# Kernel optimization log

Hardware: AMD Instinct MI355X
Metric: run time of the kernel (lower is better)

The kernel has to match this reference:

```python
import jax, jax.numpy as jnp
import numpy as np

B, S, V, E, P, C = 256, 128, 32000, 300, 200, 3
DIST_CUTOFF = 10

def _seq_mask(x):
    # TF: count_nonzero over seq, sequence_mask, expand to [B, S, 1]
    size = jnp.sum(x != 0, axis=1)
    m = (jnp.arange(S)[None, :] < size[:, None]).astype(jnp.float32)
    return m[:, :, None]

def _l2norm(w):
    n = jnp.sqrt(jnp.maximum(jnp.sum(w * w, axis=-1, keepdims=True), 1e-12))
    return w / n

def setup_inputs() -> dict:
    key = jax.random.key(0)
    ks = jax.random.split(key, 11)
    std = 0.01
    x1 = jax.random.randint(ks[0], (B, S), 0, V, dtype=jnp.int32)
    x2 = jax.random.randint(ks[1], (B, S), 0, V, dtype=jnp.int32)
    emb = jax.random.normal(ks[2], (V, E), jnp.float32)
    w_intra = jax.random.normal(ks[3], (E, E), jnp.float32) * std
    bias_intra = jax.random.normal(ks[4], (1,), jnp.float32) * std
    w_proj1 = jax.random.normal(ks[5], (2 * E, P), jnp.float32) * std
    w_proj2 = jax.random.normal(ks[6], (2 * E, P), jnp.float32) * std
    w_att = jax.random.normal(ks[7], (P, P), jnp.float32) * std
    w_cmp1 = jax.random.normal(ks[8], (2 * P, 2 * P), jnp.float32) * std
    w_cmp2 = jax.random.normal(ks[9], (2 * P, 2 * P), jnp.float32) * std
    w_agg = jax.random.normal(ks[10], (4 * P, C), jnp.float32) * std
    return dict(x1=x1, x2=x2, emb=emb, w_intra=w_intra, bias_intra=bias_intra,
                w_proj1=w_proj1, w_proj2=w_proj2, w_att=w_att,
                w_cmp1=w_cmp1, w_cmp2=w_cmp2, w_agg=w_agg)

def reference(x1, x2, emb, w_intra, bias_intra, w_proj1, w_proj2, w_att, w_cmp1, w_cmp2, w_agg):
    relu = jax.nn.relu
    mask1, mask2 = _seq_mask(x1), _seq_mask(x2)  # [B,S,1]

    # normalized embedding lookup
    e = _l2norm(emb)
    e1, e2 = e[x1], e[x2]  # [B,S,E]

    # intra-attention with distance bias (bias zeroed for |i-j| < 10)
    idx = jnp.arange(S)
    dist = jnp.abs(idx[None, :] - idx[:, None])
    dbias = bias_intra[0] * (dist >= DIST_CUTOFF).astype(jnp.float32)  # [S,S]

    def intra(x):
        f = relu(x @ w_intra)                       # shared F, [B,S,E]
        att = jnp.einsum('bik,bjk->bij', f, f)      # [B,S,S]
        sm = jax.nn.softmax(att + dbias[None], axis=2)
        xp = jnp.einsum('bik,bkj->bij', sm, x)
        return jnp.concatenate([x, xp], axis=2)     # [B,S,2E]

    e1, e2 = intra(e1), intra(e2)

    # project
    x1p = relu(e1 @ w_proj1)  # [B,S,P]
    x2p = relu(e2 @ w_proj2)

    # attend: F(x1) . F(x2), multiplicative mask, two softmaxes
    f1 = relu(x1p @ w_att)
    f2 = relu(x2p @ w_att)
    sim = jnp.einsum('bik,bjk->bij', f1, f2)          # [B,S1,S2]
    sim = sim * (mask1 * jnp.swapaxes(mask2, 1, 2))   # multiplicative mask (as in source)
    alpha = jnp.einsum('bki,bkj->bij', jax.nn.softmax(sim, axis=1), x1p)  # [B,S2,P]
    beta = jnp.einsum('bik,bkj->bij', jax.nn.softmax(sim, axis=2), x2p)   # [B,S1,P]

    # compare
    v1 = relu(jnp.concatenate([x1p, beta], axis=2) @ w_cmp1)
    v2 = relu(jnp.concatenate([x2p, alpha], axis=2) @ w_cmp2)

    # aggregate (masked sum pooling) + final ReLU projection (faithful to source)
    v1 = jnp.sum(v1 * mask1, axis=1)
    v2 = jnp.sum(v2 * mask2, axis=1)
    y_hat = relu(jnp.concatenate([v1, v2], axis=1) @ w_agg)  # [B,C]
    return y_hat
```

## Files before the change

### kernel.cpp

```cpp
#include <hip/hip_runtime.h>

#define BATCH 256
#define SEQ   128
#define EDIM  300
#define PDIM  200
#define BSTOK (BATCH * SEQ)

#define F_RELU  1
#define F_ACCUM 2

typedef unsigned short u16;
typedef __attribute__((ext_vector_type(8))) short bf16x8;
typedef __attribute__((ext_vector_type(4))) float f32x4;

__device__ __forceinline__ u16 f2bf(float x) {
    unsigned u = __float_as_uint(x);
    unsigned r = u + 0x7fffu + ((u >> 16) & 1u);
    return (u16)(r >> 16);
}
__device__ __forceinline__ float bf2f(u16 h) {
    return __uint_as_float(((unsigned)h) << 16);
}

__device__ __forceinline__ void split_store(const float* va, u16* dH, u16* dL)
{
    unsigned hp[8], lp[8];
    #pragma unroll
    for (int i = 0; i < 8; i++) {
        const unsigned u0 = __float_as_uint(va[2 * i]);
        const unsigned u1 = __float_as_uint(va[2 * i + 1]);
        const unsigned h0 = u0 & 0xffff0000u;
        const unsigned h1 = u1 & 0xffff0000u;
        hp[i] = (u0 >> 16) | h1;
        const float r0 = va[2 * i]     - __uint_as_float(h0);
        const float r1 = va[2 * i + 1] - __uint_as_float(h1);
        lp[i] = (__float_as_uint(r0) >> 16) | (__float_as_uint(r1) & 0xffff0000u);
    }
    ((uint4*)dH)[0] = make_uint4(hp[0], hp[1], hp[2], hp[3]);
    ((uint4*)dH)[1] = make_uint4(hp[4], hp[5], hp[6], hp[7]);
    ((uint4*)dL)[0] = make_uint4(lp[0], lp[1], lp[2], lp[3]);
    ((uint4*)dL)[1] = make_uint4(lp[4], lp[5], lp[6], lp[7]);
}

__device__ __forceinline__ void hi_store(const float* va, u16* dH)
{
    unsigned hp[8];
    #pragma unroll
    for (int i = 0; i < 8; i++)
        hp[i] = (unsigned)f2bf(va[2 * i]) | ((unsigned)f2bf(va[2 * i + 1]) << 16);
    ((uint4*)dH)[0] = make_uint4(hp[0], hp[1], hp[2], hp[3]);
    ((uint4*)dH)[1] = make_uint4(hp[4], hp[5], hp[6], hp[7]);
}

__device__ __forceinline__ void load16(float* va, const float* __restrict__ src,
                                       bool row_ok, int kbase, int Kvalid)
{
    if (row_ok) {
        #pragma unroll
        for (int i = 0; i < 4; i++) {
            const float4 v = *(const float4*)(src + i * 4);
            va[i * 4 + 0] = v.x; va[i * 4 + 1] = v.y;
            va[i * 4 + 2] = v.z; va[i * 4 + 3] = v.w;
        }
        #pragma unroll
        for (int i = 0; i < 16; i++)
            va[i] = (kbase + i < Kvalid) ? va[i] : 0.f;
    } else {
        #pragma unroll
        for (int i = 0; i < 16; i++) va[i] = 0.f;
    }
}

__device__ __forceinline__ void stage16(const float* __restrict__ src, bool row_ok,
                                        int kbase, int Kvalid, u16* dH, u16* dL)
{
    float va[16];
    load16(va, src, row_ok, kbase, Kvalid);
    split_store(va, dH, dL);
}

__device__ __forceinline__ void stage16_hi(const float* __restrict__ src, bool row_ok,
                                           int kbase, int Kvalid, u16* dH)
{
    float va[16];
    load16(va, src, row_ok, kbase, Kvalid);
    hi_store(va, dH);
}

__device__ __forceinline__ void gather16(float* va, const float* __restrict__ erow,
                                         float nrm, int kb)
{
    if (kb + 16 <= EDIM) {
        #pragma unroll
        for (int i = 0; i < 4; i++) {
            const float4 v = *(const float4*)(erow + kb + i * 4);
            va[i * 4 + 0] = v.x; va[i * 4 + 1] = v.y;
            va[i * 4 + 2] = v.z; va[i * 4 + 3] = v.w;
        }
    } else {
        #pragma unroll
        for (int i = 0; i < 16; i++)
            va[i] = (kb + i < EDIM) ? erow[kb + i] : 0.f;
    }
    #pragma unroll
    for (int i = 0; i < 16; i++) va[i] *= nrm;
}

__device__ __forceinline__ void stage_gather(const float* __restrict__ erow, float nrm,
                                             int kb, u16* dH, u16* dL)
{
    float va[16];
    gather16(va, erow, nrm, kb);
    split_store(va, dH, dL);
}

__device__ __forceinline__ void stage_gather_hi(const float* __restrict__ erow, float nrm,
                                                int kb, u16* dH)
{
    float va[16];
    gather16(va, erow, nrm, kb);
    hi_store(va, dH);
}

#define MFMA3(ai, aj) \
    acc[ai][aj] = __builtin_amdgcn_mfma_f32_16x16x32_bf16(fah[ai], fbh[aj], acc[ai][aj], 0, 0, 0); \
    acc[ai][aj] = __builtin_amdgcn_mfma_f32_16x16x32_bf16(fah[ai], fbl[aj], acc[ai][aj], 0, 0, 0); \
    acc[ai][aj] = __builtin_amdgcn_mfma_f32_16x16x32_bf16(fal[ai], fbh[aj], acc[ai][aj], 0, 0, 0);

#define MFMA1(ai, aj) \
    acc[ai][aj] = __builtin_amdgcn_mfma_f32_16x16x32_bf16(fah[ai], fbh[aj], acc[ai][aj], 0, 0, 0);

__device__ __forceinline__ void store_transposed(
    float* __restrict__ PT, const f32x4 (*acc)[4], float* TR,
    int bn, int Nvalid, int wm, int wn, int lr, int quad, int tid, bool relu)
{
    #pragma unroll
    for (int h = 0; h < 2; h++) {
        __syncthreads();
        if ((wn >> 6) == h) {
            #pragma unroll
            for (int j = 0; j < 4; j++) {
                const int col = j * 16 + lr;
                #pragma unroll
                for (int i = 0; i < 4; i++)
                    #pragma unroll
                    for (int r = 0; r < 4; r++) {
                        float v = acc[i][j][r];
                        if (relu) v = fmaxf(v, 0.f);
                        TR[col * 129 + wm + i * 16 + quad * 4 + r] = v;
                    }
            }
        }
        __syncthreads();
        const int row = tid >> 2;
        const int gp = bn + h * 64 + row;
        if (gp < Nvalid) {
            float* dst = PT + (long long)gp * 128;
            for (int c = (tid & 3); c < 32; c += 4) {
                const int base = row * 129 + c * 4;
                *(float4*)(dst + c * 4) =
                    make_float4(TR[base], TR[base + 1], TR[base + 2], TR[base + 3]);
            }
        }
    }
}

__global__ __launch_bounds__(256) void gemm_proj(
    const int* __restrict__ x1, const int* __restrict__ x2,
    const float* __restrict__ emb, const float* __restrict__ norms,
    const u16* __restrict__ W1h, const u16* __restrict__ W1l,
    const u16* __restrict__ W2h, const u16* __restrict__ W2l,
    float* __restrict__ T, float* __restrict__ F0, float* __restrict__ F1)
{
    __shared__ __align__(16) unsigned char smem[40960];
    u16 (*AsH)[40] = (u16(*)[40])(smem);
    u16 (*AsL)[40] = (u16(*)[40])(smem + 10240);
    u16 (*BsH)[40] = (u16(*)[40])(smem + 20480);
    u16 (*BsL)[40] = (u16(*)[40])(smem + 30720);

    const int tid = threadIdx.x;
    const int id  = blockIdx.y * 5 + blockIdx.x;
    const int xcd = id & 7;
    const int s   = id >> 3;
    const int mt  = xcd + 8 * (s / 5);
    const int bm  = mt * 128;
    const int bn  = (s % 5) * 128;
    const bool side2 = mt >= 256;
    const bool wb = bn < 256;

    const u16* Bh = side2 ? W2h : W1h;
    const u16* Bl = side2 ? W2l : W1l;
    float* F = side2 ? F1 : F0;
    const int fm = side2 ? bm - 32768 : bm;
    const int* toks = (side2 ? x2 - 32768 : x1) + bm;

    const int wave = tid >> 6;
    const int lane = tid & 63;
    const int wm   = (wave >> 1) * 64;
    const int wn   = (wave & 1) * 64;
    const int lr   = lane & 15;
    const int quad = lane >> 4;
    const int sr   = tid >> 1;
    const int sc   = (tid & 1) * 16;

    const int tok = toks[sr];
    const float nrm = norms[tok];
    const float* erow = emb + (long long)tok * EDIM;

    f32x4 acc[4][4];
    #pragma unroll
    for (int i = 0; i < 4; i++)
        #pragma unroll
        for (int j = 0; j < 4; j++)
            acc[i][j] = (f32x4)(0.0f);

    for (int k0 = 0; k0 < 320; k0 += 32) {
        if (wb) stage_gather(erow, nrm, k0 + sc, &AsH[sr][sc], &AsL[sr][sc]);
        else    stage_gather_hi(erow, nrm, k0 + sc, &AsH[sr][sc]);
        {
            uint4 wh0 = make_uint4(0,0,0,0), wh1 = make_uint4(0,0,0,0);
            const int gn = bn + sr;
            const long long br = (long long)gn * 320 + k0 + sc;
            if (gn < 556) {
                wh0 = *(const uint4*)(Bh + br);
                wh1 = *(const uint4*)(Bh + br + 8);
            }
            *(uint4*)&BsH[sr][sc]     = wh0;
            *(uint4*)&BsH[sr][sc + 8] = wh1;
            if (wb) {
                uint4 wl0 = make_uint4(0,0,0,0), wl1 = make_uint4(0,0,0,0);
                if (gn < 556) {
                    wl0 = *(const uint4*)(Bl + br);
                    wl1 = *(const uint4*)(Bl + br + 8);
                }
                *(uint4*)&BsL[sr][sc]     = wl0;
                *(uint4*)&BsL[sr][sc + 8] = wl1;
            }
        }
        __syncthreads();

        bf16x8 fah[4], fal[4], fbh[4], fbl[4];
        #pragma unroll
        for (int i = 0; i < 4; i++) {
            fah[i] = *(const bf16x8*)&AsH[wm + i * 16 + lr][quad * 8];
            fbh[i] = *(const bf16x8*)&BsH[wn + i * 16 + lr][quad * 8];
        }
        if (wb) {
            #pragma unroll
            for (int i = 0; i < 4; i++) {
                fal[i] = *(const bf16x8*)&AsL[wm + i * 16 + lr][quad * 8];
                fbl[i] = *(const bf16x8*)&BsL[wn + i * 16 + lr][quad * 8];
            }
            #pragma unroll
            for (int i = 0; i < 4; i++)
                #pragma unroll
                for (int j = 0; j < 4; j++) { MFMA3(i, j) }
        } else {
            #pragma unroll
            for (int i = 0; i < 4; i++)
                #pragma unroll
                for (int j = 0; j < 4; j++) { MFMA1(i, j) }
        }
        __syncthreads();
    }

    if (wb) {
        float* Tb = T + (long long)mt * (PDIM * SEQ);
        store_transposed(Tb, acc, (float*)smem, bn, PDIM, wm, wn, lr, quad, tid, false);
    } else {
        #pragma unroll
        for (int i = 0; i < 4; i++) {
            #pragma unroll
            for (int j = 0; j < 4; j++) {
                const int idx = bn + wn + j * 16 + lr - 256;
                if (idx >= EDIM) continue;
                #pragma unroll
                for (int r = 0; r < 4; r++) {
                    const int gm = fm + wm + i * 16 + quad * 4 + r;
                    F[(long long)gm * EDIM + idx] = fmaxf(acc[i][j][r], 0.f);
                }
            }
        }
    }
}

__global__ __launch_bounds__(256) void gemm_xp(
    const float* __restrict__ P, float* __restrict__ T,
    const int* __restrict__ x1, const int* __restrict__ x2,
    const float* __restrict__ emb, const float* __restrict__ norms,
    const u16* __restrict__ W1h, const u16* __restrict__ W1l,
    const u16* __restrict__ W2h, const u16* __restrict__ W2l,
    float* __restrict__ XCAT)
{
    __shared__ __align__(16) unsigned char smem[40960];
    u16 (*AsH)[40] = (u16(*)[40])(smem);
    u16 (*AsL)[40] = (u16(*)[40])(smem + 10240);
    u16 (*BsH)[40] = (u16(*)[40])(smem + 20480);
    u16 (*BsL)[40] = (u16(*)[40])(smem + 30720);

    const int tid = threadIdx.x;
    const int bz  = blockIdx.z;
    const int bn  = blockIdx.x * 128;

    const int wave = tid >> 6;
    const int lane = tid & 63;
    const int wm   = (wave >> 1) * 64;
    const int wn   = (wave & 1) * 64;
    const int lr   = lane & 15;
    const int quad = lane >> 4;
    const int sr   = tid >> 1;
    const int sc   = (tid & 1) * 16;

    const int* toks = (bz < BATCH) ? x1 + bz * SEQ : x2 + (bz - BATCH) * SEQ;
    const u16* Wh = (bz < BATCH) ? W1h : W2h;
    const u16* Wl = (bz < BATCH) ? W1l : W2l;
    const int tok = toks[sr];
    const float nrm = norms[tok];
    const float* erow = emb + (long long)tok * EDIM;
    const float* Pb = P + (long long)bz * (SEQ * SEQ);
    float* Tb = T + (long long)bz * (PDIM * SEQ);

    f32x4 acc[4][4];
    #pragma unroll
    for (int i = 0; i < 4; i++)
        #pragma unroll
        for (int j = 0; j < 4; j++)
            acc[i][j] = (f32x4)(0.0f);

    for (int k0 = 0; k0 < 320; k0 += 32) {
        stage_gather(erow, nrm, k0 + sc, &AsH[sr][sc], &AsL[sr][sc]);
        {
            uint4 wh0 = make_uint4(0,0,0,0), wh1 = make_uint4(0,0,0,0);
            uint4 wl0 = make_uint4(0,0,0,0), wl1 = make_uint4(0,0,0,0);
            const int gn = bn + sr;
            if (gn < PDIM) {
                const long long br = (long long)gn * 320 + k0 + sc;
                wh0 = *(const uint4*)(Wh + br);
                wh1 = *(const uint4*)(Wh + br + 8);
                wl0 = *(const uint4*)(Wl + br);
                wl1 = *(const uint4*)(Wl + br + 8);
            }
            *(uint4*)&BsH[sr][sc]     = wh0;
            *(uint4*)&BsH[sr][sc + 8] = wh1;
            *(uint4*)&BsL[sr][sc]     = wl0;
            *(uint4*)&BsL[sr][sc + 8] = wl1;
        }
        __syncthreads();

        bf16x8 fah[4], fal[4], fbh[4], fbl[4];
        #pragma unroll
        for (int i = 0; i < 4; i++) {
            fah[i] = *(const bf16x8*)&AsH[wm + i * 16 + lr][quad * 8];
            fal[i] = *(const bf16x8*)&AsL[wm + i * 16 + lr][quad * 8];
            fbh[i] = *(const bf16x8*)&BsH[wn + i * 16 + lr][quad * 8];
            fbl[i] = *(const bf16x8*)&BsL[wn + i * 16 + lr][quad * 8];
        }
        #pragma unroll
        for (int i = 0; i < 4; i++)
            #pragma unroll
            for (int j = 0; j < 4; j++) { MFMA3(i, j) }
        __syncthreads();
    }

    for (int k0 = 0; k0 < 128; k0 += 32) {
        stage16(Pb + (long long)sr * 128 + k0 + sc, true, 0, 1 << 30,
                &AsH[sr][sc], &AsL[sr][sc]);
        const int gn = bn + sr;
        stage16(Tb + (long long)gn * 128 + k0 + sc, gn < PDIM, 0, 1 << 30,
                &BsH[sr][sc], &BsL[sr][sc]);
        __syncthreads();

        bf16x8 fah[4], fal[4], fbh[4], fbl[4];
        #pragma unroll
        for (int i = 0; i < 4; i++) {
            fah[i] = *(const bf16x8*)&AsH[wm + i * 16 + lr][quad * 8];
            fal[i] = *(const bf16x8*)&AsL[wm + i * 16 + lr][quad * 8];
            fbh[i] = *(const bf16x8*)&BsH[wn + i * 16 + lr][quad * 8];
            fbl[i] = *(const bf16x8*)&BsL[wn + i * 16 + lr][quad * 8];
        }
        #pragma unroll
        for (int i = 0; i < 4; i++)
            #pragma unroll
            for (int j = 0; j < 4; j++) { MFMA3(i, j) }
        __syncthreads();
    }

    const long long rowbase = (long long)bz * SEQ;
    #pragma unroll
    for (int i = 0; i < 4; i++) {
        #pragma unroll
        for (int j = 0; j < 4; j++) {
            const int gn = bn + wn + j * 16 + lr;
            if (gn >= PDIM) continue;
            #pragma unroll
            for (int r = 0; r < 4; r++) {
                const int gm = wm + i * 16 + quad * 4 + r;
                XCAT[(rowbase + gm) * 400 + gn] = fmaxf(acc[i][j][r], 0.f);
            }
        }
    }
    store_transposed(Tb, acc, (float*)smem, bn, PDIM, wm, wn, lr, quad, tid, true);
}

template <int NM>
__global__ __launch_bounds__(256) void gemm_flat(
    const float* __restrict__ A,
    const u16* __restrict__ Bh, const u16* __restrict__ Bl,
    const u16* __restrict__ Bh2, const u16* __restrict__ Bl2, int Msplit,
    float* __restrict__ C, float* __restrict__ PO, const int* __restrict__ sizes,
    int M, int N, int Kp, int lda, int ldb, int ldc, int flags)
{
    __shared__ u16 AsH[128][40];
    __shared__ u16 AsL[128][40];
    __shared__ u16 BsH[128][40];
    __shared__ u16 BsL[128][40];

    const int tid = threadIdx.x;
    int bx = blockIdx.x, by = blockIdx.y;
    if ((gridDim.y & 7) == 0) {
        const int gx = gridDim.x;
        const int id = by * gx + bx;
        const int xcd = id & 7;
        const int s = id >> 3;
        by = xcd + 8 * (s / gx);
        bx = s % gx;
    }
    const int bm = by * 128;
    const int bn = bx * 128;

    const int wave = tid >> 6;
    const int lane = tid & 63;
    const int wm   = (wave >> 1) * 64;
    const int wn   = (wave & 1) * 64;
    const int lr   = lane & 15;
    const int quad = lane >> 4;
    const int sr   = tid >> 1;
    const int sc   = (tid & 1) * 16;

    if (bm >= Msplit) { Bh = Bh2; Bl = Bl2; }

    f32x4 acc[4][4];
    #pragma unroll
    for (int i = 0; i < 4; i++)
        #pragma unroll
        for (int j = 0; j < 4; j++)
            acc[i][j] = (f32x4)(0.0f);

    for (int k0 = 0; k0 < Kp; k0 += 32) {
        if constexpr (NM == 3)
            stage16(A + (long long)(bm + sr) * lda + k0 + sc, true, 0, 1 << 30,
                    &AsH[sr][sc], &AsL[sr][sc]);
        else
            stage16_hi(A + (long long)(bm + sr) * lda + k0 + sc, true, 0, 1 << 30,
                       &AsH[sr][sc]);
        {
            uint4 wh0 = make_uint4(0,0,0,0), wh1 = make_uint4(0,0,0,0);
            const int gn = bn + sr;
            const long long br = (long long)gn * ldb + k0 + sc;
            if (gn < N) {
                wh0 = *(const uint4*)(Bh + br);
                wh1 = *(const uint4*)(Bh + br + 8);
            }
            *(uint4*)&BsH[sr][sc]     = wh0;
            *(uint4*)&BsH[sr][sc + 8] = wh1;
            if constexpr (NM == 3) {
                uint4 wl0 = make_uint4(0,0,0,0), wl1 = make_uint4(0,0,0,0);
                if (gn < N) {
                    wl0 = *(const uint4*)(Bl + br);
                    wl1 = *(const uint4*)(Bl + br + 8);
                }
                *(uint4*)&BsL[sr][sc]     = wl0;
                *(uint4*)&BsL[sr][sc + 8] = wl1;
            }
        }
        __syncthreads();

        bf16x8 fah[4], fal[4], fbh[4], fbl[4];
        #pragma unroll
        for (int i = 0; i < 4; i++) {
            fah[i] = *(const bf16x8*)&AsH[wm + i * 16 + lr][quad * 8];
            fbh[i] = *(const bf16x8*)&BsH[wn + i * 16 + lr][quad * 8];
        }
        if constexpr (NM == 3) {
            #pragma unroll
            for (int i = 0; i < 4; i++) {
                fal[i] = *(const bf16x8*)&AsL[wm + i * 16 + lr][quad * 8];
                fbl[i] = *(const bf16x8*)&BsL[wn + i * 16 + lr][quad * 8];
            }
            #pragma unroll
            for (int i = 0; i < 4; i++)
                #pragma unroll
                for (int j = 0; j < 4; j++) { MFMA3(i, j) }
        } else {
            #pragma unroll
            for (int i = 0; i < 4; i++)
                #pragma unroll
                for (int j = 0; j < 4; j++) { MFMA1(i, j) }
        }
        __syncthreads();
    }

    const int sz = PO ? sizes[bm >> 7] : 0;
    float ps[4] = {0.f, 0.f, 0.f, 0.f};
    #pragma unroll
    for (int j = 0; j < 4; j++) {
        const int gn = bn + wn + j * 16 + lr;
        const bool gok = gn < N;
        #pragma unroll
        for (int i = 0; i < 4; i++) {
            #pragma unroll
            for (int r = 0; r < 4; r++) {
                const int row = wm + i * 16 + quad * 4 + r;
                const int gm = bm + row;
                float v = acc[i][j][r];
                if (flags & F_RELU) v = fmaxf(v, 0.f);
                if (gok && C) C[(long long)gm * ldc + gn] = v;
                if (PO && row < sz) ps[j] += v;
            }
        }
    }
    if (PO) {
        #pragma unroll
        for (int j = 0; j < 4; j++) {
            ps[j] += __shfl_xor(ps[j], 16);
            ps[j] += __shfl_xor(ps[j], 32);
        }
        float* PS = (float*)AsH;
        if (wm == 0 && quad == 0) {
            #pragma unroll
            for (int j = 0; j < 4; j++) PS[wn + j * 16 + lr] = ps[j];
        }
        __syncthreads();
        if (wm == 64 && quad == 0) {
            #pragma unroll
            for (int j = 0; j < 4; j++) PS[wn + j * 16 + lr] += ps[j];
        }
        __syncthreads();
        if (tid < 128) {
            const int gn = bn + tid;
            if (gn < N) PO[(long long)(bm >> 7) * N + gn] = PS[tid];
        }
    }
}

template <int MODE>
__global__ __launch_bounds__(256) void gemm_bat(
    const float* __restrict__ A, const float* __restrict__ Aalt,
    const float* __restrict__ B, const float* __restrict__ Balt,
    float* __restrict__ C, float* __restrict__ PT,
    int N, int Kvalid, int Kp, int lda, int ldb, int ldc,
    long long sA, long long sB, long long sC, long long sPT,
    int flags, const float* __restrict__ bias_ptr, const int* __restrict__ sizes,
    int same_ab)
{
    constexpr int NM = (MODE == 0) ? 3 : 1;
    constexpr int SB = (MODE >= 1) ? 65536 : 40960;
    __shared__ __align__(16) unsigned char smem[SB];
    u16 (*AsH)[40] = (u16(*)[40])(smem);
    u16 (*AsL)[40] = (u16(*)[40])(smem + 10240);
    u16 (*BsH)[40] = (u16(*)[40])(smem + 20480);
    u16 (*BsL)[40] = (u16(*)[40])(smem + 30720);

    const int bz = blockIdx.z;
    long long zb = bz;
    const float* Ause = A;
    const float* Buse = B;
    if (Aalt && bz >= BATCH) { Ause = Aalt; Buse = Balt; zb = bz - BATCH; }
    Ause += zb * sA;
    Buse += zb * sB;
    C += (long long)bz * sC;
    if (PT) PT += (long long)bz * sPT;

    const int tid  = threadIdx.x;
    const int bn   = blockIdx.x * 128;
    const int wave = tid >> 6;
    const int lane = tid & 63;
    const int wm   = (wave >> 1) * 64;
    const int wn   = (wave & 1) * 64;
    const int lr   = lane & 15;
    const int quad = lane >> 4;
    const int sr   = tid >> 1;
    const int sc   = (tid & 1) * 16;

    f32x4 acc[4][4];
    #pragma unroll
    for (int i = 0; i < 4; i++)
        #pragma unroll
        for (int j = 0; j < 4; j++)
            acc[i][j] = (f32x4)(0.0f);

    u16 (*fbH)[40] = same_ab ? AsH : BsH;
    u16 (*fbL)[40] = same_ab ? AsL : BsL;

    for (int k0 = 0; k0 < Kp; k0 += 32) {
        if constexpr (NM == 3)
            stage16(Ause + (long long)sr * lda + k0 + sc, true, k0 + sc, Kvalid,
                    &AsH[sr][sc], &AsL[sr][sc]);
        else
            stage16_hi(Ause + (long long)sr * lda + k0 + sc, true, k0 + sc, Kvalid,
                       &AsH[sr][sc]);
        if (!same_ab) {
            const int gn = bn + sr;
            if constexpr (NM == 3)
                stage16(Buse + (long long)gn * ldb + k0 + sc, gn < N, k0 + sc, Kvalid,
                        &BsH[sr][sc], &BsL[sr][sc]);
            else
                stage16_hi(Buse + (long long)gn * ldb + k0 + sc, gn < N, k0 + sc, Kvalid,
                           &BsH[sr][sc]);
        }
        __syncthreads();

        bf16x8 fah[4], fal[4], fbh[4], fbl[4];
        #pragma unroll
        for (int i = 0; i < 4; i++) {
            fah[i] = *(const bf16x8*)&AsH[wm + i * 16 + lr][quad * 8];
            fbh[i] = *(const bf16x8*)&fbH[wn + i * 16 + lr][quad * 8];
        }
        if constexpr (NM == 3) {
            #pragma unroll
            for (int i = 0; i < 4; i++) {
                fal[i] = *(const bf16x8*)&AsL[wm + i * 16 + lr][quad * 8];
                fbl[i] = *(const bf16x8*)&fbL[wn + i * 16 + lr][quad * 8];
            }
            #pragma unroll
            for (int i = 0; i < 4; i++)
                #pragma unroll
                for (int j = 0; j < 4; j++) { MFMA3(i, j) }
        } else {
            #pragma unroll
            for (int i = 0; i < 4; i++)
                #pragma unroll
                for (int j = 0; j < 4; j++) { MFMA1(i, j) }
        }
        __syncthreads();
    }

    if (MODE == 1) {
        float* S = (float*)smem;
        const float bias = bias_ptr[0];
        #pragma unroll
        for (int i = 0; i < 4; i++) {
            #pragma unroll
            for (int j = 0; j < 4; j++) {
                const int col = wn + j * 16 + lr;
                #pragma unroll
                for (int r = 0; r < 4; r++) {
                    const int row = wm + i * 16 + quad * 4 + r;
                    int d = row - col; d = d < 0 ? -d : d;
                    S[row * 128 + col] = acc[i][j][r] + ((d >= 10) ? bias : 0.f);
                }
            }
        }
        __syncthreads();
        const int row = tid >> 1;
        const int half = (tid & 1) * 64;
        float mx = -1e30f;
        for (int c = 0; c < 64; c++) mx = fmaxf(mx, S[row * 128 + half + c]);
        mx = fmaxf(mx, __shfl_xor(mx, 1));
        float sum = 0.f;
        for (int c = 0; c < 64; c++) sum += __expf(S[row * 128 + half + c] - mx);
        sum += __shfl_xor(sum, 1);
        const float inv = 1.f / sum;
        for (int c = 0; c < 64; c++)
            C[(long long)row * ldc + half + c] = __expf(S[row * 128 + half + c] - mx) * inv;
    } else if (MODE == 2) {
        float* S = (float*)smem;
        const int s1 = sizes[bz];
        const int s2 = sizes[BATCH + bz];
        #pragma unroll
        for (int i = 0; i < 4; i++) {
            #pragma unroll
            for (int j = 0; j < 4; j++) {
                const int col = wn + j * 16 + lr;
                #pragma unroll
                for (int r = 0; r < 4; r++) {
                    const int row = wm + i * 16 + quad * 4 + r;
                    float v = acc[i][j][r];
                    if (row >= s1 || col >= s2) v = 0.f;
                    S[row * 128 + col] = v;
                }
            }
        }
        __syncthreads();
        const int idx = tid >> 1;
        const int half = (tid & 1) * 64;
        {
            float mx = -1e30f;
            for (int c = 0; c < 64; c++) mx = fmaxf(mx, S[idx * 128 + half + c]);
            mx = fmaxf(mx, __shfl_xor(mx, 1));
            float sum = 0.f;
            for (int c = 0; c < 64; c++) sum += __expf(S[idx * 128 + half + c] - mx);
            sum += __shfl_xor(sum, 1);
            const float inv = 1.f / sum;
            for (int c = 0; c < 64; c++)
                C[(long long)idx * 128 + half + c] = __expf(S[idx * 128 + half + c] - mx) * inv;
        }
        {
            float mx = -1e30f;
            for (int r = 0; r < 64; r++) mx = fmaxf(mx, S[(half + r) * 128 + idx]);
            mx = fmaxf(mx, __shfl_xor(mx, 1));
            float sum = 0.f;
            for (int r = 0; r < 64; r++) sum += __expf(S[(half + r) * 128 + idx] - mx);
            sum += __shfl_xor(sum, 1);
            const float inv = 1.f / sum;
            for (int r = 0; r < 64; r++)
                PT[(long long)idx * 128 + half + r] = __expf(S[(half + r) * 128 + idx] - mx) * inv;
        }
    } else {
        const int s1 = sizes ? sizes[bz] : SEQ;
        const int s2 = sizes ? sizes[BATCH + bz] : SEQ;
        #pragma unroll
        for (int i = 0; i < 4; i++) {
            #pragma unroll
            for (int j = 0; j < 4; j++) {
                const int gn = bn + wn + j * 16 + lr;
                if (gn >= N) continue;
                #pragma unroll
                for (int r = 0; r < 4; r++) {
                    const int gm = wm + i * 16 + quad * 4 + r;
                    float v = acc[i][j][r];
                    if (sizes && (gm >= s1 || gn >= s2)) v = 0.f;
                    if (flags & F_ACCUM) v += C[(long long)gm * ldc + gn];
                    if (flags & F_RELU)  v = fmaxf(v, 0.f);
                    C[(long long)gm * ldc + gn] = v;
                    if (PT) PT[(long long)gn * 128 + gm] = v;
                }
            }
        }
    }
}

struct WEnt { const float* src; u16* H; u16* L; int K, N, Kp, rowStart; };
struct WTab { WEnt e[11]; };
__global__ void convert_all(WTab t)
{
    const int row = blockIdx.y;
    const int k = blockIdx.x * 256 + threadIdx.x;
    #pragma unroll
    for (int s = 0; s < 11; s++) {
        const WEnt w = t.e[s];
        if (row >= w.rowStart && row < w.rowStart + w.N) {
            const int n = row - w.rowStart;
            if (k < w.Kp) {
                const float v = (k < w.K) ? w.src[(long long)k * w.N + n] : 0.f;
                const u16 h = f2bf(v);
                w.H[(long long)n * w.Kp + k] = h;
                w.L[(long long)n * w.Kp + k] = f2bf(v - bf2f(h));
            }
            return;
        }
    }
}

__global__ void norms_kernel(const float* __restrict__ emb, float* __restrict__ norms)
{
    const int r = blockIdx.x;
    const int lane = threadIdx.x;
    const float* row = emb + (long long)r * EDIM;
    float ss = 0.f;
    #pragma unroll
    for (int i = 0; i < 5; i++) {
        const int c = lane + i * 64;
        const float f = (c < EDIM) ? row[c] : 0.f;
        ss += f * f;
    }
    #pragma unroll
    for (int o = 32; o > 0; o >>= 1) ss += __shfl_xor(ss, o);
    if (lane == 0) norms[r] = rsqrtf(fmaxf(ss, 1e-12f));
}

__global__ void sizes_kernel(const int* __restrict__ x1, const int* __restrict__ x2,
                             int* __restrict__ sizes)
{
    const int b = blockIdx.x;
    const int side = blockIdx.y;
    const int* x = (side ? x2 : x1) + b * SEQ;
    const int nz = (x[threadIdx.x] != 0) ? 1 : 0;
    const unsigned long long bal = __ballot(nz);
    __shared__ int part[2];
    if ((threadIdx.x & 63) == 0) part[threadIdx.x >> 6] = __popcll(bal);
    __syncthreads();
    if (threadIdx.x == 0) sizes[side * BATCH + b] = part[0] + part[1];
}

__global__ void agg_kernel(const float* __restrict__ v1s, const float* __restrict__ v2s,
                           const float* __restrict__ w_agg, float* __restrict__ y)
{
    const int b = blockIdx.x;
    const int lane = threadIdx.x;
    float a0 = 0.f, a1 = 0.f, a2 = 0.f;
    for (int k = lane; k < 800; k += 64) {
        const float v = (k < 400) ? v1s[b * 400 + k] : v2s[b * 400 + k - 400];
        a0 = fmaf(v, w_agg[k * 3 + 0], a0);
        a1 = fmaf(v, w_agg[k * 3 + 1], a1);
        a2 = fmaf(v, w_agg[k * 3 + 2], a2);
    }
    #pragma unroll
    for (int o = 32; o > 0; o >>= 1) {
        a0 += __shfl_xor(a0, o);
        a1 += __shfl_xor(a1, o);
        a2 += __shfl_xor(a2, o);
    }
    if (lane == 0) {
        y[b * 3 + 0] = fmaxf(a0, 0.f);
        y[b * 3 + 1] = fmaxf(a1, 0.f);
        y[b * 3 + 2] = fmaxf(a2, 0.f);
    }
}

extern "C" void kernel_launch(void* const* d_in, const int* in_sizes, int n_in,
                              void* d_out, int out_size, void* d_ws, size_t ws_size,
                              hipStream_t stream)
{
    (void)in_sizes; (void)n_in; (void)out_size; (void)ws_size;
    const int*   x1         = (const int*)d_in[0];
    const int*   x2         = (const int*)d_in[1];
    const float* emb        = (const float*)d_in[2];
    const float* w_intra    = (const float*)d_in[3];
    const float* bias_intra = (const float*)d_in[4];
    const float* w_proj1    = (const float*)d_in[5];
    const float* w_proj2    = (const float*)d_in[6];
    const float* w_att      = (const float*)d_in[7];
    const float* w_cmp1     = (const float*)d_in[8];
    const float* w_cmp2     = (const float*)d_in[9];
    const float* w_agg      = (const float*)d_in[10];
    float* y  = (float*)d_out;
    float* ws = (float*)d_ws;

    float* X1CAT = ws;
    float* X2CAT = X1CAT + 13107200;
    float* T     = X2CAT + 13107200;
    float* FBUF  = T + 13107200;
    float* ATT   = FBUF + 9830400;
    float* POOL  = ATT + 8388608;
    int*   SIZES = (int*)(POOL + 204800);
    float* NORMS = (float*)(SIZES + 512);
    u16*   W1H   = (u16*)(NORMS + 32768);
    u16*   W1L   = W1H + 177920;
    u16*   W2H   = W1L + 177920;
    u16*   W2L   = W2H + 177920;
    u16*   WAH   = W2L + 177920;
    u16*   WAL   = WAH + 44800;
    u16*   WC1H  = WAL + 44800;
    u16*   WC1L  = WC1H + 166400;
    u16*   WC2H  = WC1L + 166400;
    u16*   WC2L  = WC2H + 166400;
    u16*   WPA1H = WC2L + 166400;
    u16*   WPA1L = WPA1H + 64000;
    u16*   WPA2H = WPA1L + 64000;
    u16*   WPA2L = WPA2H + 64000;

    float* F1X = X1CAT;
    float* F12 = FBUF;
    float* F2  = FBUF + 6553600;
    float* SIMP = F2;
    float* SMTP = F12;
    float* T1  = T;
    float* T2  = T + 6553600;

    const long long sbSS = (long long)SEQ * SEQ;
    const long long sbF  = (long long)SEQ * EDIM;
    const long long sbFP = 25600;
    const long long sbC  = (long long)SEQ * 400;
    const long long sbT  = (long long)PDIM * SEQ;

    sizes_kernel<<<dim3(BATCH, 2), 128, 0, stream>>>(x1, x2, SIZES);
    norms_kernel<<<32000, 64, 0, stream>>>(emb, NORMS);

    {
        WTab t;
        t.e[0]  = { w_proj1 + 300 * 200, W1H,             W1L,             300, 200, 320, 0    };
        t.e[1]  = { w_intra,             W1H + 200 * 320, W1L + 200 * 320,   0,  56, 320, 200  };
        t.e[2]  = { w_intra,             W1H + 256 * 320, W1L + 256 * 320, 300, 300, 320, 256  };
        t.e[3]  = { w_proj2 + 300 * 200, W2H,             W2L,             300, 200, 320, 556  };
        t.e[4]  = { w_intra,             W2H + 200 * 320, W2L + 200 * 320,   0,  56, 320, 756  };
        t.e[5]  = { w_intra,             W2H + 256 * 320, W2L + 256 * 320, 300, 300, 320, 812  };
        t.e[6]  = { w_att,               WAH,             WAL,             200, 200, 224, 1112 };
        t.e[7]  = { w_cmp1,              WC1H,            WC1L,            400, 400, 416, 1312 };
        t.e[8]  = { w_cmp2,              WC2H,            WC2L,            400, 400, 416, 1712 };
        t.e[9]  = { w_proj1,             WPA1H,           WPA1L,           300, 200, 320, 2112 };
        t.e[10] = { w_proj2,             WPA2H,           WPA2L,           300, 200, 320, 2312 };
        convert_all<<<dim3(2, 2512), 256, 0, stream>>>(t);
    }

    gemm_proj<<<dim3(5, 512), 256, 0, stream>>>(
        x1, x2, emb, NORMS, W1H, W1L, W2H, W2L, T, FBUF, F1X);
    gemm_bat<1><<<dim3(1, 1, 2 * BATCH), 256, 0, stream>>>(
        FBUF, F1X, FBUF, nullptr, ATT, nullptr,
        SEQ, EDIM, 320, EDIM, EDIM, SEQ, sbF, sbF, sbSS, 0,
        0, bias_intra, nullptr, 1);
    gemm_xp<<<dim3(2, 1, 2 * BATCH), 256, 0, stream>>>(
        ATT, T, x1, x2, emb, NORMS, WPA1H, WPA1L, WPA2H, WPA2L, X1CAT);

    gemm_flat<1><<<dim3(2, 512), 256, 0, stream>>>(
        X1CAT, WAH, WAL, WAH, WAL, 1 << 30, F12, nullptr, nullptr,
        2 * BSTOK, PDIM, 224, 400, 224, PDIM, F_RELU);
    gemm_bat<2><<<dim3(1, 1, BATCH), 256, 0, stream>>>(
        F12, nullptr, F2, nullptr, SIMP, SMTP,
        SEQ, PDIM, 224, PDIM, PDIM, SEQ, sbFP, sbFP, sbFP, sbFP,
        0, nullptr, SIZES, 0);
    gemm_bat<0><<<dim3(2, 1, 2 * BATCH), 256, 0, stream>>>(
        SIMP, SMTP, T2, T1, X1CAT + 200, nullptr,
        PDIM, SEQ, SEQ, SEQ, SEQ, 400, sbFP, sbT, sbC, 0,
        0, nullptr, nullptr, 0);

    gemm_flat<3><<<dim3(4, 512), 256, 0, stream>>>(
        X1CAT, WC1H, WC1L, WC2H, WC2L, BSTOK,
        nullptr, POOL, SIZES,
        2 * BSTOK, 400, 416, 400, 416, 400, F_RELU);
    agg_kernel<<<BATCH, 64, 0, stream>>>(POOL, POOL + 102400, w_agg, y);
}
```

Measured before the change: 551.9 us.

## Store intra-attention and attend features as padded bf16 for batched GEMM staging

The producer kernels now write the ReLU feature matrices (intra F and attend F1/F2) as bf16 into zero-padded buffers with 320 and 224 columns, replacing fp32. The batched GEMMs that consume them get a bf16 source path that copies 16-byte vectors straight into shared memory, with no fp32 load, rounding, padding checks or hi/lo split. This halves intermediate write and read traffic and simplifies staging. The workspace is re-laid out to hold the new buffers, and the sim outputs move to a dedicated region with their own stride.

New measurement: 557.5 us. About the same (+1.0%).

```diff
diff --git a/kernel.cpp b/kernel.cpp
--- a/kernel.cpp
+++ b/kernel.cpp
@@ -87,6 +87,18 @@
     hi_store(va, dH);
 }
 
+__device__ __forceinline__ void stage16_u16(const u16* __restrict__ src, bool row_ok,
+                                            u16* dH)
+{
+    uint4 a = make_uint4(0, 0, 0, 0), b = make_uint4(0, 0, 0, 0);
+    if (row_ok) {
+        a = *(const uint4*)(src);
+        b = *(const uint4*)(src + 8);
+    }
+    ((uint4*)dH)[0] = a;
+    ((uint4*)dH)[1] = b;
+}
+
 __device__ __forceinline__ void gather16(float* va, const float* __restrict__ erow,
                                          float nrm, int kb)
 {
@@ -170,7 +182,7 @@
     const float* __restrict__ emb, const float* __restrict__ norms,
     const u16* __restrict__ W1h, const u16* __restrict__ W1l,
     const u16* __restrict__ W2h, const u16* __restrict__ W2l,
-    float* __restrict__ T, float* __restrict__ F0, float* __restrict__ F1)
+    float* __restrict__ T, u16* __restrict__ F0, u16* __restrict__ F1)
 {
     __shared__ __align__(16) unsigned char smem[40960];
     u16 (*AsH)[40] = (u16(*)[40])(smem);
@@ -190,7 +202,7 @@
 
     const u16* Bh = side2 ? W2h : W1h;
     const u16* Bl = side2 ? W2l : W1l;
-    float* F = side2 ? F1 : F0;
+    u16* F = side2 ? F1 : F0;
     const int fm = side2 ? bm - 32768 : bm;
     const int* toks = (side2 ? x2 - 32768 : x1) + bm;
 
@@ -273,11 +285,13 @@
             #pragma unroll
             for (int j = 0; j < 4; j++) {
                 const int idx = bn + wn + j * 16 + lr - 256;
-                if (idx >= EDIM) continue;
+                if (idx >= 320) continue;
                 #pragma unroll
                 for (int r = 0; r < 4; r++) {
                     const int gm = fm + wm + i * 16 + quad * 4 + r;
-                    F[(long long)gm * EDIM + idx] = fmaxf(acc[i][j][r], 0.f);
+                    u16 o = 0;
+                    if (idx < EDIM) o = f2bf(fmaxf(acc[i][j][r], 0.f));
+                    F[(long long)gm * 320 + idx] = o;
                 }
             }
         }
@@ -407,7 +421,8 @@
     const float* __restrict__ A,
     const u16* __restrict__ Bh, const u16* __restrict__ Bl,
     const u16* __restrict__ Bh2, const u16* __restrict__ Bl2, int Msplit,
-    float* __restrict__ C, float* __restrict__ PO, const int* __restrict__ sizes,
+    float* __restrict__ C, u16* __restrict__ C16, int ldc16, int npad,
+    float* __restrict__ PO, const int* __restrict__ sizes,
     int M, int N, int Kp, int lda, int ldb, int ldc, int flags)
 {
     __shared__ u16 AsH[128][40];
@@ -515,6 +530,10 @@
                 float v = acc[i][j][r];
                 if (flags & F_RELU) v = fmaxf(v, 0.f);
                 if (gok && C) C[(long long)gm * ldc + gn] = v;
+                if (C16 && gn < npad) {
+                    u16 o = gok ? f2bf(v) : (u16)0;
+                    C16[(long long)gm * ldc16 + gn] = o;
+                }
                 if (PO && row < sz) ps[j] += v;
             }
         }
@@ -543,10 +562,10 @@
     }
 }
 
-template <int MODE>
+template <int MODE, bool SRC16>
 __global__ __launch_bounds__(256) void gemm_bat(
-    const float* __restrict__ A, const float* __restrict__ Aalt,
-    const float* __restrict__ B, const float* __restrict__ Balt,
+    const void* __restrict__ A, const void* __restrict__ Aalt,
+    const void* __restrict__ B, const void* __restrict__ Balt,
     float* __restrict__ C, float* __restrict__ PT,
     int N, int Kvalid, int Kp, int lda, int ldb, int ldc,
     long long sA, long long sB, long long sC, long long sPT,
@@ -563,11 +582,9 @@
 
     const int bz = blockIdx.z;
     long long zb = bz;
-    const float* Ause = A;
-    const float* Buse = B;
-    if (Aalt && bz >= BATCH) { Ause = Aalt; Buse = Balt; zb = bz - BATCH; }
-    Ause += zb * sA;
-    Buse += zb * sB;
+    const void* Araw = A;
+    const void* Braw = B;
+    if (Aalt && bz >= BATCH) { Araw = Aalt; Braw = Balt; zb = bz - BATCH; }
     C += (long long)bz * sC;
     if (PT) PT += (long long)bz * sPT;
 
@@ -593,20 +610,32 @@
     u16 (*fbL)[40] = same_ab ? AsL : BsL;
 
     for (int k0 = 0; k0 < Kp; k0 += 32) {
-        if constexpr (NM == 3)
-            stage16(Ause + (long long)sr * lda + k0 + sc, true, k0 + sc, Kvalid,
-                    &AsH[sr][sc], &AsL[sr][sc]);
-        else
-            stage16_hi(Ause + (long long)sr * lda + k0 + sc, true, k0 + sc, Kvalid,
-                       &AsH[sr][sc]);
-        if (!same_ab) {
-            const int gn = bn + sr;
+        if constexpr (SRC16) {
+            const u16* A16 = (const u16*)Araw + zb * sA;
+            stage16_u16(A16 + (long long)sr * lda + k0 + sc, true, &AsH[sr][sc]);
+            if (!same_ab) {
+                const u16* B16 = (const u16*)Braw + zb * sB;
+                const int gn = bn + sr;
+                stage16_u16(B16 + (long long)gn * ldb + k0 + sc, gn < N, &BsH[sr][sc]);
+            }
+        } else {
+            const float* Af = (const float*)Araw + zb * sA;
             if constexpr (NM == 3)
-                stage16(Buse + (long long)gn * ldb + k0 + sc, gn < N, k0 + sc, Kvalid,
-                        &BsH[sr][sc], &BsL[sr][sc]);
+                stage16(Af + (long long)sr * lda + k0 + sc, true, k0 + sc, Kvalid,
+                        &AsH[sr][sc], &AsL[sr][sc]);
             else
-                stage16_hi(Buse + (long long)gn * ldb + k0 + sc, gn < N, k0 + sc, Kvalid,
-                           &BsH[sr][sc]);
+                stage16_hi(Af + (long long)sr * lda + k0 + sc, true, k0 + sc, Kvalid,
+                           &AsH[sr][sc]);
+            if (!same_ab) {
+                const float* Bf = (const float*)Braw + zb * sB;
+                const int gn = bn + sr;
+                if constexpr (NM == 3)
+                    stage16(Bf + (long long)gn * ldb + k0 + sc, gn < N, k0 + sc, Kvalid,
+                            &BsH[sr][sc], &BsL[sr][sc]);
+                else
+                    stage16_hi(Bf + (long long)gn * ldb + k0 + sc, gn < N, k0 + sc, Kvalid,
+                               &BsH[sr][sc]);
+            }
         }
         __syncthreads();
 
@@ -830,9 +859,11 @@
     float* X1CAT = ws;
     float* X2CAT = X1CAT + 13107200;
     float* T     = X2CAT + 13107200;
-    float* FBUF  = T + 13107200;
-    float* ATT   = FBUF + 9830400;
-    float* POOL  = ATT + 8388608;
+    float* ATT   = T + 13107200;
+    u16*   FBU16 = (u16*)(ATT + 8388608);
+    u16*   F1U16 = FBU16 + 10485760;
+    u16*   F12U16= FBU16;
+    float* POOL  = (float*)(F1U16 + 10485760);
     int*   SIZES = (int*)(POOL + 204800);
     float* NORMS = (float*)(SIZES + 512);
     u16*   W1H   = (u16*)(NORMS + 32768);
@@ -850,17 +881,15 @@
     u16*   WPA2H = WPA1L + 64000;
     u16*   WPA2L = WPA2H + 64000;
 
-    float* F1X = X1CAT;
-    float* F12 = FBUF;
-    float* F2  = FBUF + 6553600;
-    float* SIMP = F2;
-    float* SMTP = F12;
-    float* T1  = T;
-    float* T2  = T + 6553600;
+    u16*   F2U16 = F12U16 + 32768 * 224;
+    float* SIMP  = ATT;
+    float* SMTP  = ATT + 4194304;
+    float* T1    = T;
+    float* T2    = T + 6553600;
 
     const long long sbSS = (long long)SEQ * SEQ;
-    const long long sbF  = (long long)SEQ * EDIM;
-    const long long sbFP = 25600;
+    const long long sbF16= 128LL * 320;
+    const long long sbP16= 128LL * 224;
     const long long sbC  = (long long)SEQ * 400;
     const long long sbT  = (long long)PDIM * SEQ;
 
@@ -884,29 +913,30 @@
     }
 
     gemm_proj<<<dim3(5, 512), 256, 0, stream>>>(
-        x1, x2, emb, NORMS, W1H, W1L, W2H, W2L, T, FBUF, F1X);
-    gemm_bat<1><<<dim3(1, 1, 2 * BATCH), 256, 0, stream>>>(
-        FBUF, F1X, FBUF, nullptr, ATT, nullptr,
-        SEQ, EDIM, 320, EDIM, EDIM, SEQ, sbF, sbF, sbSS, 0,
+        x1, x2, emb, NORMS, W1H, W1L, W2H, W2L, T, FBU16, F1U16);
+    gemm_bat<1, true><<<dim3(1, 1, 2 * BATCH), 256, 0, stream>>>(
+        FBU16, F1U16, FBU16, nullptr, ATT, nullptr,
+        SEQ, EDIM, 320, 320, 320, SEQ, sbF16, sbF16, sbSS, 0,
         0, bias_intra, nullptr, 1);
     gemm_xp<<<dim3(2, 1, 2 * BATCH), 256, 0, stream>>>(
         ATT, T, x1, x2, emb, NORMS, WPA1H, WPA1L, WPA2H, WPA2L, X1CAT);
 
     gemm_flat<1><<<dim3(2, 512), 256, 0, stream>>>(
-        X1CAT, WAH, WAL, WAH, WAL, 1 << 30, F12, nullptr, nullptr,
+        X1CAT, WAH, WAL, WAH, WAL, 1 << 30,
+        nullptr, F12U16, 224, 224, nullptr, nullptr,
         2 * BSTOK, PDIM, 224, 400, 224, PDIM, F_RELU);
-    gemm_bat<2><<<dim3(1, 1, BATCH), 256, 0, stream>>>(
-        F12, nullptr, F2, nullptr, SIMP, SMTP,
-        SEQ, PDIM, 224, PDIM, PDIM, SEQ, sbFP, sbFP, sbFP, sbFP,
+    gemm_bat<2, true><<<dim3(1, 1, BATCH), 256, 0, stream>>>(
+        F12U16, nullptr, F2U16, nullptr, SIMP, SMTP,
+        SEQ, PDIM, 224, 224, 224, SEQ, sbP16, sbP16, sbSS, sbSS,
         0, nullptr, SIZES, 0);
-    gemm_bat<0><<<dim3(2, 1, 2 * BATCH), 256, 0, stream>>>(
+    gemm_bat<0, false><<<dim3(2, 1, 2 * BATCH), 256, 0, stream>>>(
         SIMP, SMTP, T2, T1, X1CAT + 200, nullptr,
-        PDIM, SEQ, SEQ, SEQ, SEQ, 400, sbFP, sbT, sbC, 0,
+        PDIM, SEQ, SEQ, SEQ, SEQ, 400, sbSS, sbT, sbC, 0,
         0, nullptr, nullptr, 0);
 
     gemm_flat<3><<<dim3(4, 512), 256, 0, stream>>>(
         X1CAT, WC1H, WC1L, WC2H, WC2L, BSTOK,
-        nullptr, POOL, SIZES,
+        nullptr, nullptr, 0, 0, POOL, SIZES,
         2 * BSTOK, 400, 416, 400, 416, 400, F_RELU);
     agg_kernel<<<BATCH, 64, 0, stream>>>(POOL, POOL + 102400, w_agg, y);
 }
```
